# Performance work log

Hardware: AMD Instinct MI355X
Metric: run time of the kernel (lower is better)

The kernel has to match this reference:

```python
import jax, jax.numpy as jnp
import numpy as np

NF = 128   # n_feature
NA = 200000  # n_atoms
B = 256    # n_molecules (batch_mask rows)


def setup_inputs() -> dict:
    key = jax.random.key(0)
    ks = jax.random.split(key, 20)
    p = lambda k, shape: jax.random.normal(k, shape, jnp.float32) * 0.05
    s = jax.random.normal(ks[0], (1, NA, NF), jnp.float32)
    v = jax.random.normal(ks[1], (1, NA, 3, NF), jnp.float32)
    pos = jax.random.normal(ks[2], (1, NA, 3), jnp.float32)
    # one-hot batch mask: each atom assigned to one of B molecules
    idx = jax.random.randint(ks[3], (NA,), 0, B)
    batch = (idx[None, :] == jnp.arange(B)[:, None]).astype(jnp.float32)[..., None]  # (B, NA, 1)
    inp = dict(s=s, v=v, pos=pos, batch=batch)
    i = 4
    for l in range(2):  # n_output = 2 GatedEquivariant blocks
        inp[f"u{l}_w"] = p(ks[i], (NF, NF)); i += 1
        inp[f"v{l}_w"] = p(ks[i], (NF, NF)); i += 1
        inp[f"a{l}_w1"] = p(ks[i], (NF, 2 * NF)); i += 1
        inp[f"a{l}_b1"] = p(ks[i], (NF,)); i += 1
        inp[f"a{l}_w2"] = p(ks[i], (2 * NF, NF)); i += 1
        inp[f"a{l}_b2"] = p(ks[i], (2 * NF,)); i += 1
    inp["out_w"] = p(ks[i], (1, NF)); i += 1
    inp["out_b"] = p(ks[i], (1,))
    return inp


def _gated(s, v, uw, vw, aw1, ab1, aw2, ab2):
    # v: (1, na, 3, f); nn.Linear acts on last dim with weight (out, in)
    v1 = jnp.einsum('banf,gf->bang', v, uw)
    v2 = jnp.einsum('banf,gf->bang', v, vw)
    norm = jnp.linalg.norm(v2 + 1e-8, ord=2, axis=-2)  # (1, na, f)
    h = jnp.concatenate([s, norm], axis=-1)            # (1, na, 2f)
    h = jax.nn.silu(h @ aw1.T + ab1) @ aw2.T + ab2     # (1, na, 2f)
    sg, ss = jnp.split(h, 2, axis=-1)
    return sg, v1 * ss[:, :, None, :]


def reference(s, v, pos, batch,
              u0_w, v0_w, a0_w1, a0_b1, a0_w2, a0_b2,
              u1_w, v1_w, a1_w1, a1_b1, a1_w2, a1_b2,
              out_w, out_b):
    s, v = _gated(s, v, u0_w, v0_w, a0_w1, a0_b1, a0_w2, a0_b2)
    s, v = _gated(s, v, u1_w, v1_w, a1_w1, a1_b1, a1_w2, a1_b2)
    s = s @ out_w.T + out_b  # (1, na, 1)
    # faithful dense broadcast-mask pooling: (B, na, 1) * (B, na, 1) summed over atoms
    y = (jnp.broadcast_to(s, (batch.shape[0],) + s.shape[1:]) * batch).sum(axis=-2)
    return y  # (B, 1)
```

## Files before the change

kernel.cpp:

```cpp
#include <hip/hip_runtime.h>
#include <hip/hip_bf16.h>
#include <math.h>

typedef __attribute__((ext_vector_type(4))) float  f32x4;
typedef __attribute__((ext_vector_type(8))) __bf16 bf16x8;
typedef __attribute__((ext_vector_type(4))) unsigned int u32x4;

__device__ __forceinline__ f32x4 MF(bf16x8 a, bf16x8 b, f32x4 c) {
    return __builtin_amdgcn_mfma_f32_16x16x32_bf16(a, b, c, 0, 0, 0);
}

__device__ __forceinline__ f32x4 zero4() { f32x4 z = {0.f, 0.f, 0.f, 0.f}; return z; }

__device__ __forceinline__ unsigned int pkbf(float lo, float hi) {
    unsigned int r;
    asm("v_cvt_pk_bf16_f32 %0, %1, %2" : "=v"(r) : "v"(lo), "v"(hi));
    return r;
}
__device__ __forceinline__ unsigned long long pk4(f32x4 x) {
    return (unsigned long long)pkbf(x[0], x[1]) | ((unsigned long long)pkbf(x[2], x[3]) << 32);
}

__device__ __forceinline__ bf16x8 bfrag_g(const float* W, int ldk, int row, int k0) {
    const float* p = W + (size_t)row * ldk + k0;
    bf16x8 r;
#pragma unroll
    for (int e = 0; e < 8; ++e) r[e] = (__bf16)p[e];
    return r;
}

#define VSET     18432
#define SET_SZ   28672
#define RAW(b)   ((b) * SET_SZ)
#define HB(b)    ((b) * SET_SZ + VSET)
#define S1_OFF   57344
#define RED_OFF  63488
#define LDS_BYTES 64000

__device__ __forceinline__ bf16x8 ld16(const unsigned char* p, int imm) {
    return __builtin_bit_cast(bf16x8, *(const u32x4*)(p + imm));
}

__global__ __launch_bounds__(512, 2) void eqsc_main(
    const float* __restrict__ S, const float* __restrict__ V,
    const float* __restrict__ u0w, const float* __restrict__ v0w,
    const float* __restrict__ a0w1, const float* __restrict__ a0b1,
    const float* __restrict__ a0w2, const float* __restrict__ a0b2,
    const float* __restrict__ u1w, const float* __restrict__ v1w,
    const float* __restrict__ a1w1, const float* __restrict__ a1b1,
    const float* __restrict__ a1w2, const float* __restrict__ a1b2,
    const float* __restrict__ outw, const float* __restrict__ outbp,
    float* __restrict__ sOut, int NT)
{
    __shared__ __align__(16) unsigned char lds[LDS_BYTES];
    const int tid  = threadIdx.x;
    const int lane = tid & 63;
    const int wv   = tid >> 6;
    const int l15  = lane & 15;
    const int lg   = lane >> 4;
    const int grow = wv * 16 + l15;
    const int fb0  = wv * 16 + (lg << 2);

    const int lgsw    = (lg + (l15 & 7)) << 4;
    const int lrow384 = l15 * 384 + lgsw;
    const int lrow640 = l15 * 640 + lgsw;
    const int erot    = (fb0 << 1) + ((l15 & 7) << 4);
    const int eoffV   = l15 * 384 + erot;
    const int eoffH   = l15 * 640 + erot;

    int vstoff[3], sstoff;
#pragma unroll
    for (int j = 0; j < 3; ++j) {
        int c = tid + (j << 9);
        int d = c >> 9, rem = c & 511;
        int row = rem >> 5, c4 = rem & 31;
        vstoff[j] = d * 6144 + row * 384 + (c4 << 3) + ((row & 7) << 4);
    }
    { int row = tid >> 5, c4 = tid & 31;
      sstoff = row * 640 + (c4 << 3) + ((row & 7) << 4); }

    f32x4 wfv = zero4();
    float cf = 0.f;
    for (int g = 0; g < 128; ++g) {
        float og = outw[g];
        f32x4 w4 = *(const f32x4*)(a1w2 + g * 128 + fb0);
#pragma unroll
        for (int e = 0; e < 4; ++e) wfv[e] += w4[e] * og;
        cf += a1b2[g] * og;
    }
    cf += outbp[0];

    bf16x8 uw0f[4], vw0f[4], w2g0[4], w2s0[4], vw1f[4];
    bf16x8 w1f0[8], w1f1[8];
#pragma unroll
    for (int kt = 0; kt < 4; ++kt) {
        int k0 = kt * 32 + lg * 8;
        uw0f[kt] = bfrag_g(u0w, 128, grow, k0);
        vw0f[kt] = bfrag_g(v0w, 128, grow, k0);
        w2g0[kt] = bfrag_g(a0w2, 128, grow, k0);
        w2s0[kt] = bfrag_g(a0w2, 128, 128 + grow, k0);
        vw1f[kt] = bfrag_g(v1w, 128, grow, k0);
    }
#pragma unroll
    for (int kt = 0; kt < 8; ++kt) {
        int k0 = kt * 32 + lg * 8;
        w1f0[kt] = bfrag_g(a0w1, 256, grow, k0);
        w1f1[kt] = bfrag_g(a1w1, 256, grow, k0);
    }
    const f32x4 b1_0v = *(const f32x4*)(a0b1 + fb0);
    const f32x4 b2g0v = *(const f32x4*)(a0b2 + fb0);
    const f32x4 b2s0v = *(const f32x4*)(a0b2 + 128 + fb0);
    const f32x4 b1_1v = *(const f32x4*)(a1b1 + fb0);

    const int stride = gridDim.x;
    const int t0 = blockIdx.x;

    if (t0 < NT) {
        f32x4 vld[3], sld;
#pragma unroll
        for (int j = 0; j < 3; ++j) {
            int c = tid + (j << 9);
            int d = c >> 9, rem = c & 511;
            int row = rem >> 5, c4 = rem & 31;
            vld[j] = *(const f32x4*)(V + (((size_t)((t0 << 4) + row) * 3 + d) << 7) + (c4 << 2));
        }
        { int row = tid >> 5, c4 = tid & 31;
          sld = *(const f32x4*)(S + (((size_t)((t0 << 4) + row)) << 7) + (c4 << 2)); }
#pragma unroll
        for (int j = 0; j < 3; ++j)
            *(unsigned long long*)(lds + RAW(0) + vstoff[j]) = pk4(vld[j]);
        *(unsigned long long*)(lds + HB(0) + sstoff) = pk4(sld);
    }
    __syncthreads();

    int i = 0;
    for (int ty = t0; ty < NT + stride; ty += stride, ++i) {
        const bool yv = (ty < NT);
        const bool xv = (i > 0);
        const int  tz = ty + stride;
        const bool zv = (tz < NT);
        unsigned char* baseY = lds + (i & 1) * SET_SZ;
        unsigned char* baseX = lds + ((i & 1) ^ 1) * SET_SZ;
        const unsigned char* pVY = baseY + lrow384;
        const unsigned char* pHY = baseY + VSET + lrow640;
        const unsigned char* pVX = baseX + lrow384;
        const unsigned char* pHX = baseX + VSET + lrow640;
        const unsigned char* pS1 = lds + S1_OFF + lrow384;

        f32x4 vld[3], sld;
        if (zv) {
#pragma unroll
            for (int j = 0; j < 3; ++j) {
                int c = tid + (j << 9);
                int d = c >> 9, rem = c & 511;
                int row = rem >> 5, c4 = rem & 31;
                vld[j] = *(const f32x4*)(V + (((size_t)((tz << 4) + row) * 3 + d) << 7) + (c4 << 2));
            }
            { int row = tid >> 5, c4 = tid & 31;
              sld = *(const f32x4*)(S + (((size_t)((tz << 4) + row)) << 7) + (c4 << 2)); }
        }

        f32x4 v1a[3];
        if (yv) {
            f32x4 n2 = zero4();
#pragma unroll
            for (int d = 0; d < 3; ++d) {
                f32x4 a1 = zero4(), a2 = zero4();
#pragma unroll
                for (int kt = 0; kt < 4; ++kt) {
                    bf16x8 a = ld16(pVY, d * 6144 + kt * 64);
                    a1 = MF(uw0f[kt], a, a1);
                    a2 = MF(vw0f[kt], a, a2);
                }
                v1a[d] = a1;
#pragma unroll
                for (int e = 0; e < 4; ++e) { float x = a2[e] + 1e-8f; n2[e] += x * x; }
            }
            f32x4 nr;
#pragma unroll
            for (int e = 0; e < 4; ++e) nr[e] = sqrtf(n2[e]);
            *(unsigned long long*)(baseY + VSET + eoffH + 256) = pk4(nr);
        }
        if (xv) {
            f32x4 n2 = zero4();
#pragma unroll
            for (int d = 0; d < 3; ++d) {
                f32x4 acc = zero4();
#pragma unroll
                for (int kt = 0; kt < 4; ++kt)
                    acc = MF(vw1f[kt], ld16(pVX, d * 6144 + kt * 64), acc);
#pragma unroll
                for (int e = 0; e < 4; ++e) { float x = acc[e] + 1e-8f; n2[e] += x * x; }
            }
            f32x4 nr;
#pragma unroll
            for (int e = 0; e < 4; ++e) nr[e] = sqrtf(n2[e]);
            *(unsigned long long*)(baseX + VSET + eoffH + 256) = pk4(nr);
        }
        __syncthreads();

        if (yv) {
            f32x4 m = zero4();
#pragma unroll
            for (int kt = 0; kt < 8; ++kt)
                m = MF(w1f0[kt], ld16(pHY, kt * 64), m);
            f32x4 y;
#pragma unroll
            for (int e = 0; e < 4; ++e) {
                float x = m[e] + b1_0v[e];
                y[e] = x / (1.f + __expf(-x));
            }
            *(unsigned long long*)(lds + S1_OFF + eoffV) = pk4(y);
        }
        if (xv) {
            f32x4 m = zero4();
#pragma unroll
            for (int kt = 0; kt < 8; ++kt)
                m = MF(w1f1[kt], ld16(pHX, kt * 64), m);
            float p = 0.f;
#pragma unroll
            for (int e = 0; e < 4; ++e) {
                float x = m[e] + b1_1v[e];
                p += (x / (1.f + __expf(-x))) * wfv[e];
            }
            p += __shfl_xor(p, 16);
            p += __shfl_xor(p, 32);
            if (lane < 16)
                *((float*)(lds + RED_OFF) + (wv << 4) + lane) = p;
        }
        if (zv) {
#pragma unroll
            for (int j = 0; j < 3; ++j)
                *(unsigned long long*)(baseX + vstoff[j]) = pk4(vld[j]);
        }
        __syncthreads();

        if (yv) {
            f32x4 sg = zero4(), ssa = zero4();
#pragma unroll
            for (int kt = 0; kt < 4; ++kt) {
                bf16x8 a = ld16(pS1, kt * 64);
                sg  = MF(w2g0[kt], a, sg);
                ssa = MF(w2s0[kt], a, ssa);
            }
            f32x4 g, ssv;
#pragma unroll
            for (int e = 0; e < 4; ++e) {
                g[e]   = sg[e] + b2g0v[e];
                ssv[e] = ssa[e] + b2s0v[e];
            }
            *(unsigned long long*)(baseY + VSET + eoffH) = pk4(g);
#pragma unroll
            for (int d = 0; d < 3; ++d) {
                f32x4 vp;
#pragma unroll
                for (int e = 0; e < 4; ++e) vp[e] = v1a[d][e] * ssv[e];
                *(unsigned long long*)(baseY + d * 6144 + eoffV) = pk4(vp);
            }
        }
        if (zv)
            *(unsigned long long*)(baseX + VSET + sstoff) = pk4(sld);
        if (xv && tid < 16) {
            float s = 0.f;
#pragma unroll
            for (int w = 0; w < 8; ++w) s += *((float*)(lds + RED_OFF) + (w << 4) + tid);
            sOut[((ty - stride) << 4) + tid] = s + cf;
        }
        __syncthreads();
    }
}

__global__ __launch_bounds__(256) void eqsc_pool(const float* __restrict__ batch,
                                                 const float* __restrict__ s,
                                                 float* __restrict__ out,
                                                 int NA, int B, int CH)
{
    int b  = blockIdx.x % B;
    int ch = blockIdx.x / B;
    int a0 = ch * CH;
    int a1 = min(a0 + CH, NA);
    const float* br = batch + (size_t)b * NA;
    float acc = 0.f;
    for (int a = a0 + (threadIdx.x << 2); a < a1; a += 256 * 4) {
        f32x4 bb = *(const f32x4*)(br + a);
        f32x4 sv = *(const f32x4*)(s + a);
        acc += bb[0] * sv[0] + bb[1] * sv[1] + bb[2] * sv[2] + bb[3] * sv[3];
    }
#pragma unroll
    for (int off = 32; off > 0; off >>= 1) acc += __shfl_down(acc, off);
    __shared__ float wsum[4];
    if ((threadIdx.x & 63) == 0) wsum[threadIdx.x >> 6] = acc;
    __syncthreads();
    if (threadIdx.x == 0) atomicAdd(&out[b], wsum[0] + wsum[1] + wsum[2] + wsum[3]);
}

extern "C" void kernel_launch(void* const* d_in, const int* in_sizes, int n_in,
                              void* d_out, int out_size, void* d_ws, size_t ws_size,
                              hipStream_t stream)
{
    const float* S     = (const float*)d_in[0];
    const float* V     = (const float*)d_in[1];
    const float* batch = (const float*)d_in[3];
    const float* u0w   = (const float*)d_in[4];
    const float* v0w   = (const float*)d_in[5];
    const float* a0w1  = (const float*)d_in[6];
    const float* a0b1  = (const float*)d_in[7];
    const float* a0w2  = (const float*)d_in[8];
    const float* a0b2  = (const float*)d_in[9];
    const float* u1w   = (const float*)d_in[10];
    const float* v1w   = (const float*)d_in[11];
    const float* a1w1  = (const float*)d_in[12];
    const float* a1b1  = (const float*)d_in[13];
    const float* a1w2  = (const float*)d_in[14];
    const float* a1b2  = (const float*)d_in[15];
    const float* outw  = (const float*)d_in[16];
    const float* outb  = (const float*)d_in[17];

    const int NA = in_sizes[0] / 128;
    const int NT = NA / 16;
    const int B  = in_sizes[3] / NA;
    float* sAtom = (float*)d_ws;

    hipMemsetAsync(d_out, 0, (size_t)out_size * sizeof(float), stream);

    eqsc_main<<<256, 512, 0, stream>>>(S, V, u0w, v0w, a0w1, a0b1, a0w2, a0b2,
                                       u1w, v1w, a1w1, a1b1, a1w2, a1b2,
                                       outw, outb, sAtom, NT);

    const int CH  = 16384;
    const int NCH = (NA + CH - 1) / CH;
    eqsc_pool<<<B * NCH, 256, 0, stream>>>(batch, sAtom, (float*)d_out, NA, B, CH);
}
```

Before: 245.1 us.

## Fuse batch-mask pooling into main kernel with per-block LDS accumulators

Removes the separate pooling kernel and the per-atom scalar workspace round trip. Each block now loads its 16-atom slice of the batch mask for all 256 molecules one stage after computing the atom outputs, accumulates the dot products into an LDS array of per-molecule partial sums, and does one atomicAdd per molecule at the end. This saves a kernel launch and the global write and read of per-atom scalars. In exchange it adds a third pipeline stage, more registers and LDS, and many scattered 32-byte loads of the mask inside the main loop.

```diff
diff --git a/kernel.cpp b/kernel.cpp
--- a/kernel.cpp
+++ b/kernel.cpp
@@ -31,11 +31,11 @@
 
 #define VSET     18432
 #define SET_SZ   28672
-#define RAW(b)   ((b) * SET_SZ)
-#define HB(b)    ((b) * SET_SZ + VSET)
 #define S1_OFF   57344
 #define RED_OFF  63488
-#define LDS_BYTES 64000
+#define SVAL_OFF 64000
+#define YL_OFF   64064
+#define LDS_BYTES 65088
 
 __device__ __forceinline__ bf16x8 ld16(const unsigned char* p, int imm) {
     return __builtin_bit_cast(bf16x8, *(const u32x4*)(p + imm));
@@ -43,14 +43,15 @@
 
 __global__ __launch_bounds__(512, 2) void eqsc_main(
     const float* __restrict__ S, const float* __restrict__ V,
+    const float* __restrict__ batch,
     const float* __restrict__ u0w, const float* __restrict__ v0w,
     const float* __restrict__ a0w1, const float* __restrict__ a0b1,
     const float* __restrict__ a0w2, const float* __restrict__ a0b2,
-    const float* __restrict__ u1w, const float* __restrict__ v1w,
+    const float* __restrict__ v1w,
     const float* __restrict__ a1w1, const float* __restrict__ a1b1,
-    const float* __restrict__ a1w2, const float* __restrict__ a1b2,
+    const float* __restrict__ a1w2,  const float* __restrict__ a1b2,
     const float* __restrict__ outw, const float* __restrict__ outbp,
-    float* __restrict__ sOut, int NT)
+    float* __restrict__ Y, int NT, int NA, int B)
 {
     __shared__ __align__(16) unsigned char lds[LDS_BYTES];
     const int tid  = threadIdx.x;
@@ -114,8 +115,15 @@
 
     const int stride = gridDim.x;
     const int t0 = blockIdx.x;
-
-    if (t0 < NT) {
+    const int NI = (NT - t0 + stride - 1) / stride;
+
+    float* yl = (float*)(lds + YL_OFF);
+    float* sv = (float*)(lds + SVAL_OFF);
+    const int pb   = tid >> 1;
+    const int palo = (tid & 1) << 3;
+    f32x4 bb0, bb1;
+
+    {
         f32x4 vld[3], sld;
 #pragma unroll
         for (int j = 0; j < 3; ++j) {
@@ -128,17 +136,19 @@
           sld = *(const f32x4*)(S + (((size_t)((t0 << 4) + row)) << 7) + (c4 << 2)); }
 #pragma unroll
         for (int j = 0; j < 3; ++j)
-            *(unsigned long long*)(lds + RAW(0) + vstoff[j]) = pk4(vld[j]);
-        *(unsigned long long*)(lds + HB(0) + sstoff) = pk4(sld);
+            *(unsigned long long*)(lds + vstoff[j]) = pk4(vld[j]);
+        *(unsigned long long*)(lds + VSET + sstoff) = pk4(sld);
+        if (tid < 256) yl[tid] = 0.f;
     }
     __syncthreads();
 
-    int i = 0;
-    for (int ty = t0; ty < NT + stride; ty += stride, ++i) {
-        const bool yv = (ty < NT);
-        const bool xv = (i > 0);
+    for (int i = 0; i < NI + 2; ++i) {
+        const int  ty = t0 + i * stride;
+        const bool yv = (i < NI);
+        const bool xv = (i >= 1) && (i - 1 < NI);
+        const bool cv = (i >= 2) && (i - 2 < NI);
+        const bool zv = (i + 1 < NI);
         const int  tz = ty + stride;
-        const bool zv = (tz < NT);
         unsigned char* baseY = lds + (i & 1) * SET_SZ;
         unsigned char* baseX = lds + ((i & 1) ^ 1) * SET_SZ;
         const unsigned char* pVY = baseY + lrow384;
@@ -159,6 +169,15 @@
             { int row = tid >> 5, c4 = tid & 31;
               sld = *(const f32x4*)(S + (((size_t)((tz << 4) + row)) << 7) + (c4 << 2)); }
         }
+        if (cv) {
+            float p = 0.f;
+#pragma unroll
+            for (int k = 0; k < 4; ++k) p += bb0[k] * sv[palo + k];
+#pragma unroll
+            for (int k = 0; k < 4; ++k) p += bb1[k] * sv[palo + 4 + k];
+            p += __shfl_xor(p, 1);
+            if (!(tid & 1)) yl[pb] += p;
+        }
 
         f32x4 v1a[3];
         if (yv) {
@@ -199,6 +218,11 @@
         }
         __syncthreads();
 
+        if (xv) {
+            const float* bp = batch + (size_t)pb * NA + (((size_t)(ty - stride)) << 4) + palo;
+            bb0 = *(const f32x4*)bp;
+            bb1 = *(const f32x4*)(bp + 4);
+        }
         if (yv) {
             f32x4 m = zero4();
 #pragma unroll
@@ -264,34 +288,12 @@
             float s = 0.f;
 #pragma unroll
             for (int w = 0; w < 8; ++w) s += *((float*)(lds + RED_OFF) + (w << 4) + tid);
-            sOut[((ty - stride) << 4) + tid] = s + cf;
+            sv[tid] = s + cf;
         }
         __syncthreads();
     }
-}
-
-__global__ __launch_bounds__(256) void eqsc_pool(const float* __restrict__ batch,
-                                                 const float* __restrict__ s,
-                                                 float* __restrict__ out,
-                                                 int NA, int B, int CH)
-{
-    int b  = blockIdx.x % B;
-    int ch = blockIdx.x / B;
-    int a0 = ch * CH;
-    int a1 = min(a0 + CH, NA);
-    const float* br = batch + (size_t)b * NA;
-    float acc = 0.f;
-    for (int a = a0 + (threadIdx.x << 2); a < a1; a += 256 * 4) {
-        f32x4 bb = *(const f32x4*)(br + a);
-        f32x4 sv = *(const f32x4*)(s + a);
-        acc += bb[0] * sv[0] + bb[1] * sv[1] + bb[2] * sv[2] + bb[3] * sv[3];
-    }
-#pragma unroll
-    for (int off = 32; off > 0; off >>= 1) acc += __shfl_down(acc, off);
-    __shared__ float wsum[4];
-    if ((threadIdx.x & 63) == 0) wsum[threadIdx.x >> 6] = acc;
-    __syncthreads();
-    if (threadIdx.x == 0) atomicAdd(&out[b], wsum[0] + wsum[1] + wsum[2] + wsum[3]);
+
+    if (tid < B) atomicAdd(&Y[tid], yl[tid]);
 }
 
 extern "C" void kernel_launch(void* const* d_in, const int* in_sizes, int n_in,
@@ -307,7 +309,6 @@
     const float* a0b1  = (const float*)d_in[7];
     const float* a0w2  = (const float*)d_in[8];
     const float* a0b2  = (const float*)d_in[9];
-    const float* u1w   = (const float*)d_in[10];
     const float* v1w   = (const float*)d_in[11];
     const float* a1w1  = (const float*)d_in[12];
     const float* a1b1  = (const float*)d_in[13];
@@ -319,15 +320,10 @@
     const int NA = in_sizes[0] / 128;
     const int NT = NA / 16;
     const int B  = in_sizes[3] / NA;
-    float* sAtom = (float*)d_ws;
 
     hipMemsetAsync(d_out, 0, (size_t)out_size * sizeof(float), stream);
 
-    eqsc_main<<<256, 512, 0, stream>>>(S, V, u0w, v0w, a0w1, a0b1, a0w2, a0b2,
-                                       u1w, v1w, a1w1, a1b1, a1w2, a1b2,
-                                       outw, outb, sAtom, NT);
-
-    const int CH  = 16384;
-    const int NCH = (NA + CH - 1) / CH;
-    eqsc_pool<<<B * NCH, 256, 0, stream>>>(batch, sAtom, (float*)d_out, NA, B, CH);
-}
+    eqsc_main<<<256, 512, 0, stream>>>(S, V, batch, u0w, v0w, a0w1, a0b1, a0w2, a0b2,
+                                       v1w, a1w1, a1b1, a1w2, a1b2,
+                                       outw, outb, (float*)d_out, NT, NA, B);
+}
```

After: 251.5 us. +2.6%, slower.
